# Performance work log

Hardware: AMD Instinct MI355X
Metric: run time of the kernel (lower is better)

Reference implementation:

```python
import jax, jax.numpy as jnp
import numpy as np

B, L, ATTN, HID = 1024, 512, 1000, 1000

def setup_inputs() -> dict:
    key = jax.random.key(0)
    k = jax.random.split(key, 5)
    return {
        "hc": jax.random.normal(k[0], (B, HID), dtype=jnp.float32),
        "ho": jax.random.normal(k[1], (B, L, ATTN), dtype=jnp.float32),
        "mask": jnp.zeros((B, L), dtype=bool),
        "Wa_w": jax.random.normal(k[2], (1, ATTN), dtype=jnp.float32) / np.sqrt(ATTN),
        "Wa_b": jnp.zeros((1,), dtype=jnp.float32),
        "Wc_w": jax.random.normal(k[3], (HID, HID + ATTN), dtype=jnp.float32) / np.sqrt(HID + ATTN),
        "Wc_b": jnp.zeros((HID,), dtype=jnp.float32),
    }

def reference(hc, ho, mask, Wa_w, Wa_b, Wc_w, Wc_b):
    # scores: Wa(ho) -> [B, L], then mask + softmax over L
    scores = jnp.einsum('bld,od->bl', ho, Wa_w) + Wa_b[0]
    scores = jnp.where(mask, -10000.0, scores)
    a = jax.nn.softmax(scores, axis=-1)            # [B, L]
    c = jnp.einsum('bl,bld->bd', a, ho)            # context [B, ATTN]
    # dropout in eval mode (identity); concat + output projection
    h = jnp.concatenate([hc, c], axis=1) @ Wc_w.T + Wc_b  # [B, HID]
    return h
```

## Files before the change

kernel.cpp:

```cpp
#include <hip/hip_runtime.h>

#define NB 1024
#define NL 512
#define ND 1000
#define NH 1000
#define KP 2048

typedef __attribute__((ext_vector_type(8))) short bf16x8;
typedef __attribute__((ext_vector_type(4))) float f32x4;

__device__ __forceinline__ unsigned short f2bf(float f) {
    unsigned u = __float_as_uint(f);
    u += 0x7FFFu + ((u >> 16) & 1u);
    return (unsigned short)(u >> 16);
}

__global__ __launch_bounds__(256) void prep_kernel(
    const float* __restrict__ hc, const float* __restrict__ W,
    unsigned short* __restrict__ Xb, unsigned short* __restrict__ Wb)
{
    const int bid = blockIdx.x, t = threadIdx.x;
    if (bid < NB) {
        ushort4* xq = (ushort4*)(Xb + (size_t)bid * KP);
        if (t < 250) {
            float4 v = ((const float4*)(hc + (size_t)bid * NH))[t];
            xq[t] = make_ushort4(f2bf(v.x), f2bf(v.y), f2bf(v.z), f2bf(v.w));
        } else if (t < 262) {
            xq[500 + (t - 250)] = make_ushort4(0, 0, 0, 0);
        }
    } else {
        const int n = bid - NB;
        ushort4* wq = (ushort4*)(Wb + (size_t)n * KP);
        if (n < NH) {
            #pragma unroll
            for (int rep = 0; rep < 2; ++rep) {
                int q = t + rep * 256;
                if (q < 500) {
                    float4 v = ((const float4*)(W + (size_t)n * (NH + ND)))[q];
                    wq[q] = make_ushort4(f2bf(v.x), f2bf(v.y), f2bf(v.z), f2bf(v.w));
                } else {
                    wq[q] = make_ushort4(0, 0, 0, 0);
                }
            }
        } else {
            wq[t]       = make_ushort4(0, 0, 0, 0);
            wq[t + 256] = make_ushort4(0, 0, 0, 0);
        }
    }
}

__global__ __launch_bounds__(256, 4) void attn_pool_kernel(
    const float* __restrict__ ho,
    const unsigned char* __restrict__ mask,
    const float* __restrict__ Wa_w,
    const float* __restrict__ Wa_b,
    unsigned short* __restrict__ Xb)
{
    __shared__ __align__(16) float cacc[4][ND];
    __shared__ unsigned char msk[NL];
    __shared__ float mArr[4], sArr[4];

    const int b    = blockIdx.x;
    const int tid  = threadIdx.x;
    const int wave = tid >> 6;
    const int lane = tid & 63;

    const unsigned char* mb = mask + (size_t)b * NL;
    msk[tid]       = mb[tid];
    msk[tid + 256] = mb[tid + 256];

    float4 wa[4];
    #pragma unroll
    for (int j = 0; j < 4; ++j) {
        int slot = lane + 64 * j;
        wa[j] = (slot < 250) ? ((const float4*)Wa_w)[slot] : make_float4(0.f, 0.f, 0.f, 0.f);
    }
    const float bias = Wa_b[0];

    const float4* hob = (const float4*)(ho + (size_t)b * NL * ND);

    __syncthreads();

    auto loadRow = [&](int l, float4* v) {
        const float4* rp = hob + (size_t)l * 250;
        #pragma unroll
        for (int j = 0; j < 3; ++j) v[j] = rp[lane + 64 * j];
        v[3] = (lane < 58) ? rp[lane + 192] : make_float4(0.f, 0.f, 0.f, 0.f);
    };

    float  m = -1e30f, s = 0.f;
    float4 acc[4];
    #pragma unroll
    for (int j = 0; j < 4; ++j) acc[j] = make_float4(0.f, 0.f, 0.f, 0.f);

    float4 cur[4], nx1[4], nx2[4];
    loadRow(wave, cur);
    loadRow(4 + wave, nx1);

    #pragma unroll 2
    for (int c = 0; c < 128; ++c) {
        if (c + 2 < 128) loadRow(4 * (c + 2) + wave, nx2);

        float p = 0.f;
        #pragma unroll
        for (int j = 0; j < 4; ++j)
            p += cur[j].x * wa[j].x + cur[j].y * wa[j].y +
                 cur[j].z * wa[j].z + cur[j].w * wa[j].w;
        #pragma unroll
        for (int off = 32; off > 0; off >>= 1) p += __shfl_xor(p, off, 64);

        int l = 4 * c + wave;
        float sc = p + bias;
        if (msk[l]) sc = -10000.f;

        float mn = fmaxf(m, sc);
        if (mn > m) {
            float f = __expf(m - mn);
            s *= f;
            #pragma unroll
            for (int j = 0; j < 4; ++j) {
                acc[j].x *= f; acc[j].y *= f; acc[j].z *= f; acc[j].w *= f;
            }
            m = mn;
        }
        float w = __expf(sc - m);
        s += w;
        #pragma unroll
        for (int j = 0; j < 4; ++j) {
            acc[j].x += w * cur[j].x; acc[j].y += w * cur[j].y;
            acc[j].z += w * cur[j].z; acc[j].w += w * cur[j].w;
        }

        #pragma unroll
        for (int j = 0; j < 4; ++j) { cur[j] = nx1[j]; nx1[j] = nx2[j]; }
    }

    float4* cw = (float4*)&cacc[wave][0];
    #pragma unroll
    for (int j = 0; j < 4; ++j) {
        int slot = lane + 64 * j;
        if (slot < 250) cw[slot] = acc[j];
    }
    if (lane == 0) { mArr[wave] = m; sArr[wave] = s; }
    __syncthreads();

    float gm = fmaxf(fmaxf(mArr[0], mArr[1]), fmaxf(mArr[2], mArr[3]));
    float f0 = __expf(mArr[0] - gm), f1 = __expf(mArr[1] - gm);
    float f2 = __expf(mArr[2] - gm), f3 = __expf(mArr[3] - gm);
    float S  = f0 * sArr[0] + f1 * sArr[1] + f2 * sArr[2] + f3 * sArr[3];
    float inv = 1.0f / S;

    if (tid < 250) {
        float4 a0 = ((float4*)&cacc[0][0])[tid];
        float4 a1 = ((float4*)&cacc[1][0])[tid];
        float4 a2 = ((float4*)&cacc[2][0])[tid];
        float4 a3 = ((float4*)&cacc[3][0])[tid];
        float4 r;
        r.x = (f0 * a0.x + f1 * a1.x + f2 * a2.x + f3 * a3.x) * inv;
        r.y = (f0 * a0.y + f1 * a1.y + f2 * a2.y + f3 * a3.y) * inv;
        r.z = (f0 * a0.z + f1 * a1.z + f2 * a2.z + f3 * a3.z) * inv;
        r.w = (f0 * a0.w + f1 * a1.w + f2 * a2.w + f3 * a3.w) * inv;
        ((ushort4*)(Xb + (size_t)b * KP + ND))[tid] =
            make_ushort4(f2bf(r.x), f2bf(r.y), f2bf(r.z), f2bf(r.w));
    }
}

__global__ __launch_bounds__(256, 1) void mfma_proj_kernel(
    const unsigned short* __restrict__ Xb,
    const unsigned short* __restrict__ Wb,
    const float* __restrict__ wb,
    float* __restrict__ out)
{
    __shared__ float red[64][65];

    const int tid  = threadIdx.x;
    const int wave = tid >> 6;
    const int lane = tid & 63;
    const int row0 = blockIdx.x * 64;
    const int col0 = blockIdx.y * 64;
    const int r    = lane & 15;
    const int g    = lane >> 4;

    const int kbase = wave * 512 + g * 8;
    const unsigned short* xp = Xb + (size_t)(row0 + r) * KP + kbase;
    const unsigned short* wp = Wb + (size_t)(col0 + r) * KP + kbase;

    f32x4 acc[4][4];
    #pragma unroll
    for (int mi = 0; mi < 4; ++mi)
        #pragma unroll
        for (int ni = 0; ni < 4; ++ni)
            acc[mi][ni] = (f32x4){0.f, 0.f, 0.f, 0.f};

    bf16x8 a_[4], b_[4], an[4], bn[4];
    #pragma unroll
    for (int i = 0; i < 4; ++i) {
        a_[i] = *(const bf16x8*)(xp + (size_t)i * 16 * KP);
        b_[i] = *(const bf16x8*)(wp + (size_t)i * 16 * KP);
    }

    #pragma unroll 1
    for (int ks = 0; ks < 16; ++ks) {
        if (ks + 1 < 16) {
            const unsigned short* xq = xp + (ks + 1) * 32;
            const unsigned short* wq = wp + (ks + 1) * 32;
            #pragma unroll
            for (int i = 0; i < 4; ++i) {
                an[i] = *(const bf16x8*)(xq + (size_t)i * 16 * KP);
                bn[i] = *(const bf16x8*)(wq + (size_t)i * 16 * KP);
            }
        }
        #pragma unroll
        for (int mi = 0; mi < 4; ++mi)
            #pragma unroll
            for (int ni = 0; ni < 4; ++ni)
                acc[mi][ni] = __builtin_amdgcn_mfma_f32_16x16x32_bf16(
                    a_[mi], b_[ni], acc[mi][ni], 0, 0, 0);
        #pragma unroll
        for (int i = 0; i < 4; ++i) { a_[i] = an[i]; b_[i] = bn[i]; }
    }

    #pragma unroll
    for (int w = 0; w < 4; ++w) {
        if (wave == w) {
            #pragma unroll
            for (int mi = 0; mi < 4; ++mi)
                #pragma unroll
                for (int ni = 0; ni < 4; ++ni)
                    #pragma unroll
                    for (int j = 0; j < 4; ++j) {
                        int rr = mi * 16 + g * 4 + j;
                        int cc = ni * 16 + r;
                        float v = acc[mi][ni][j];
                        if (w == 0) red[rr][cc] = v;
                        else        red[rr][cc] += v;
                    }
        }
        __syncthreads();
    }

    const int cc = tid & 63;
    const int rg = tid >> 6;
    const int gc = col0 + cc;
    if (gc < NH) {
        float bias = wb[gc];
        #pragma unroll
        for (int i = 0; i < 16; ++i) {
            int rr = rg * 16 + i;
            out[(size_t)(row0 + rr) * NH + gc] = red[rr][cc] + bias;
        }
    }
}

extern "C" void kernel_launch(void* const* d_in, const int* in_sizes, int n_in,
                              void* d_out, int out_size, void* d_ws, size_t ws_size,
                              hipStream_t stream) {
    const float* hc           = (const float*)d_in[0];
    const float* ho           = (const float*)d_in[1];
    const unsigned char* mask = (const unsigned char*)d_in[2];
    const float* Wa_w         = (const float*)d_in[3];
    const float* Wa_b         = (const float*)d_in[4];
    const float* Wc_w         = (const float*)d_in[5];
    const float* Wc_b         = (const float*)d_in[6];
    float* out = (float*)d_out;

    unsigned short* Xb = (unsigned short*)d_ws;
    unsigned short* Wb = (unsigned short*)d_ws + (size_t)NB * KP;

    prep_kernel<<<2048, 256, 0, stream>>>(hc, Wc_w, Xb, Wb);
    attn_pool_kernel<<<NB, 256, 0, stream>>>(ho, mask, Wa_w, Wa_b, Xb);
    mfma_proj_kernel<<<dim3(16, 16), 256, 0, stream>>>(Xb, Wb, Wc_b, out);
}
```

Baseline: 386.7 us.

## Fuse bf16 prep into attention kernel and retile projection GEMM to 32-row blocks

Removes the separate prep kernel and folds the hc and Wc_w bf16 conversion and padding into the attention-pooling kernel, one W row per block, saving a launch and a pass over those inputs. The projection kernel now uses 32x64 output tiles with a 512-block grid and 2 blocks per CU to raise parallelism. The serialized four-step shared-memory reduction across waves becomes per-wave buffers summed in one pass after a single barrier. The fused conversion adds work ahead of the bandwidth-bound ho streaming, and the smaller tiles load each W tile twice as often.

```diff
diff --git a/kernel.cpp b/kernel.cpp
--- a/kernel.cpp
+++ b/kernel.cpp
@@ -14,47 +14,19 @@
     u += 0x7FFFu + ((u >> 16) & 1u);
     return (unsigned short)(u >> 16);
 }
-
-__global__ __launch_bounds__(256) void prep_kernel(
-    const float* __restrict__ hc, const float* __restrict__ W,
-    unsigned short* __restrict__ Xb, unsigned short* __restrict__ Wb)
-{
-    const int bid = blockIdx.x, t = threadIdx.x;
-    if (bid < NB) {
-        ushort4* xq = (ushort4*)(Xb + (size_t)bid * KP);
-        if (t < 250) {
-            float4 v = ((const float4*)(hc + (size_t)bid * NH))[t];
-            xq[t] = make_ushort4(f2bf(v.x), f2bf(v.y), f2bf(v.z), f2bf(v.w));
-        } else if (t < 262) {
-            xq[500 + (t - 250)] = make_ushort4(0, 0, 0, 0);
-        }
-    } else {
-        const int n = bid - NB;
-        ushort4* wq = (ushort4*)(Wb + (size_t)n * KP);
-        if (n < NH) {
-            #pragma unroll
-            for (int rep = 0; rep < 2; ++rep) {
-                int q = t + rep * 256;
-                if (q < 500) {
-                    float4 v = ((const float4*)(W + (size_t)n * (NH + ND)))[q];
-                    wq[q] = make_ushort4(f2bf(v.x), f2bf(v.y), f2bf(v.z), f2bf(v.w));
-                } else {
-                    wq[q] = make_ushort4(0, 0, 0, 0);
-                }
-            }
-        } else {
-            wq[t]       = make_ushort4(0, 0, 0, 0);
-            wq[t + 256] = make_ushort4(0, 0, 0, 0);
-        }
-    }
+__device__ __forceinline__ ushort4 f2bf4(float4 v) {
+    return make_ushort4(f2bf(v.x), f2bf(v.y), f2bf(v.z), f2bf(v.w));
 }
 
 __global__ __launch_bounds__(256, 4) void attn_pool_kernel(
+    const float* __restrict__ hc,
     const float* __restrict__ ho,
     const unsigned char* __restrict__ mask,
     const float* __restrict__ Wa_w,
     const float* __restrict__ Wa_b,
-    unsigned short* __restrict__ Xb)
+    const float* __restrict__ W,
+    unsigned short* __restrict__ Xb,
+    unsigned short* __restrict__ Wb)
 {
     __shared__ __align__(16) float cacc[4][ND];
     __shared__ unsigned char msk[NL];
@@ -64,6 +36,28 @@
     const int tid  = threadIdx.x;
     const int wave = tid >> 6;
     const int lane = tid & 63;
+
+    ushort4* xq = (ushort4*)(Xb + (size_t)b * KP);
+    if (tid < 250) {
+        xq[tid] = f2bf4(((const float4*)(hc + (size_t)b * NH))[tid]);
+    } else if (tid < 262) {
+        xq[500 + (tid - 250)] = make_ushort4(0, 0, 0, 0);
+    }
+    ushort4* wq = (ushort4*)(Wb + (size_t)b * KP);
+    if (b < NH) {
+        #pragma unroll
+        for (int rep = 0; rep < 2; ++rep) {
+            int q = tid + rep * 256;
+            if (q < 500) {
+                wq[q] = f2bf4(((const float4*)(W + (size_t)b * (NH + ND)))[q]);
+            } else {
+                wq[q] = make_ushort4(0, 0, 0, 0);
+            }
+        }
+    } else {
+        wq[tid]       = make_ushort4(0, 0, 0, 0);
+        wq[tid + 256] = make_ushort4(0, 0, 0, 0);
+    }
 
     const unsigned char* mb = mask + (size_t)b * NL;
     msk[tid]       = mb[tid];
@@ -160,23 +154,22 @@
         r.y = (f0 * a0.y + f1 * a1.y + f2 * a2.y + f3 * a3.y) * inv;
         r.z = (f0 * a0.z + f1 * a1.z + f2 * a2.z + f3 * a3.z) * inv;
         r.w = (f0 * a0.w + f1 * a1.w + f2 * a2.w + f3 * a3.w) * inv;
-        ((ushort4*)(Xb + (size_t)b * KP + ND))[tid] =
-            make_ushort4(f2bf(r.x), f2bf(r.y), f2bf(r.z), f2bf(r.w));
-    }
-}
-
-__global__ __launch_bounds__(256, 1) void mfma_proj_kernel(
+        ((ushort4*)(Xb + (size_t)b * KP + ND))[tid] = f2bf4(r);
+    }
+}
+
+__global__ __launch_bounds__(256, 2) void mfma_proj_kernel(
     const unsigned short* __restrict__ Xb,
     const unsigned short* __restrict__ Wb,
     const float* __restrict__ wb,
     float* __restrict__ out)
 {
-    __shared__ float red[64][65];
+    __shared__ float red[4][32][68];
 
     const int tid  = threadIdx.x;
     const int wave = tid >> 6;
     const int lane = tid & 63;
-    const int row0 = blockIdx.x * 64;
+    const int row0 = blockIdx.x * 32;
     const int col0 = blockIdx.y * 64;
     const int r    = lane & 15;
     const int g    = lane >> 4;
@@ -185,19 +178,18 @@
     const unsigned short* xp = Xb + (size_t)(row0 + r) * KP + kbase;
     const unsigned short* wp = Wb + (size_t)(col0 + r) * KP + kbase;
 
-    f32x4 acc[4][4];
-    #pragma unroll
-    for (int mi = 0; mi < 4; ++mi)
+    f32x4 acc[2][4];
+    #pragma unroll
+    for (int mi = 0; mi < 2; ++mi)
         #pragma unroll
         for (int ni = 0; ni < 4; ++ni)
             acc[mi][ni] = (f32x4){0.f, 0.f, 0.f, 0.f};
 
-    bf16x8 a_[4], b_[4], an[4], bn[4];
-    #pragma unroll
-    for (int i = 0; i < 4; ++i) {
-        a_[i] = *(const bf16x8*)(xp + (size_t)i * 16 * KP);
-        b_[i] = *(const bf16x8*)(wp + (size_t)i * 16 * KP);
-    }
+    bf16x8 a_[2], b_[4], an[2], bn[4];
+    #pragma unroll
+    for (int i = 0; i < 2; ++i) a_[i] = *(const bf16x8*)(xp + (size_t)i * 16 * KP);
+    #pragma unroll
+    for (int i = 0; i < 4; ++i) b_[i] = *(const bf16x8*)(wp + (size_t)i * 16 * KP);
 
     #pragma unroll 1
     for (int ks = 0; ks < 16; ++ks) {
@@ -205,49 +197,41 @@
             const unsigned short* xq = xp + (ks + 1) * 32;
             const unsigned short* wq = wp + (ks + 1) * 32;
             #pragma unroll
-            for (int i = 0; i < 4; ++i) {
-                an[i] = *(const bf16x8*)(xq + (size_t)i * 16 * KP);
-                bn[i] = *(const bf16x8*)(wq + (size_t)i * 16 * KP);
-            }
-        }
-        #pragma unroll
-        for (int mi = 0; mi < 4; ++mi)
+            for (int i = 0; i < 2; ++i) an[i] = *(const bf16x8*)(xq + (size_t)i * 16 * KP);
+            #pragma unroll
+            for (int i = 0; i < 4; ++i) bn[i] = *(const bf16x8*)(wq + (size_t)i * 16 * KP);
+        }
+        #pragma unroll
+        for (int mi = 0; mi < 2; ++mi)
             #pragma unroll
             for (int ni = 0; ni < 4; ++ni)
                 acc[mi][ni] = __builtin_amdgcn_mfma_f32_16x16x32_bf16(
                     a_[mi], b_[ni], acc[mi][ni], 0, 0, 0);
         #pragma unroll
-        for (int i = 0; i < 4; ++i) { a_[i] = an[i]; b_[i] = bn[i]; }
-    }
-
-    #pragma unroll
-    for (int w = 0; w < 4; ++w) {
-        if (wave == w) {
-            #pragma unroll
-            for (int mi = 0; mi < 4; ++mi)
-                #pragma unroll
-                for (int ni = 0; ni < 4; ++ni)
-                    #pragma unroll
-                    for (int j = 0; j < 4; ++j) {
-                        int rr = mi * 16 + g * 4 + j;
-                        int cc = ni * 16 + r;
-                        float v = acc[mi][ni][j];
-                        if (w == 0) red[rr][cc] = v;
-                        else        red[rr][cc] += v;
-                    }
-        }
-        __syncthreads();
-    }
+        for (int i = 0; i < 2; ++i) a_[i] = an[i];
+        #pragma unroll
+        for (int i = 0; i < 4; ++i) b_[i] = bn[i];
+    }
+
+    #pragma unroll
+    for (int mi = 0; mi < 2; ++mi)
+        #pragma unroll
+        for (int ni = 0; ni < 4; ++ni)
+            #pragma unroll
+            for (int j = 0; j < 4; ++j)
+                red[wave][mi * 16 + g * 4 + j][ni * 16 + r] = acc[mi][ni][j];
+    __syncthreads();
 
     const int cc = tid & 63;
-    const int rg = tid >> 6;
+    const int r0 = (tid >> 6) * 8;
     const int gc = col0 + cc;
     if (gc < NH) {
-        float bias = wb[gc];
-        #pragma unroll
-        for (int i = 0; i < 16; ++i) {
-            int rr = rg * 16 + i;
-            out[(size_t)(row0 + rr) * NH + gc] = red[rr][cc] + bias;
+        float bb = wb[gc];
+        #pragma unroll
+        for (int i = 0; i < 8; ++i) {
+            int rr = r0 + i;
+            float v = red[0][rr][cc] + red[1][rr][cc] + red[2][rr][cc] + red[3][rr][cc];
+            out[(size_t)(row0 + rr) * NH + gc] = v + bb;
         }
     }
 }
@@ -267,7 +251,6 @@
     unsigned short* Xb = (unsigned short*)d_ws;
     unsigned short* Wb = (unsigned short*)d_ws + (size_t)NB * KP;
 
-    prep_kernel<<<2048, 256, 0, stream>>>(hc, Wc_w, Xb, Wb);
-    attn_pool_kernel<<<NB, 256, 0, stream>>>(ho, mask, Wa_w, Wa_b, Xb);
-    mfma_proj_kernel<<<dim3(16, 16), 256, 0, stream>>>(Xb, Wb, Wc_b, out);
-}
+    attn_pool_kernel<<<NB, 256, 0, stream>>>(hc, ho, mask, Wa_w, Wa_b, Wc_w, Xb, Wb);
+    mfma_proj_kernel<<<dim3(32, 16), 256, 0, stream>>>(Xb, Wb, Wc_b, out);
+}
```

Result: no change. 389.2 us (+0.6%).
